# Kernel tuning notes

Hardware: AMD Instinct MI355X
Metric: run time of the kernel (lower is better)

The kernel has to match this reference:

```python
import jax, jax.numpy as jnp
import numpy as np

B, L, H, NH, DH, V, NL = 256, 100, 384, 12, 32, 30000, 6
FF = 4 * H


def _gelu(x):
    c = np.sqrt(2.0 / np.pi).astype(np.float32)
    return x * (0.5 * (1.0 + jnp.tanh(c * (x + 0.044715 * x ** 3))))


def _norm(X, g, b):
    mu = jnp.mean(X, axis=2, keepdims=True)
    var = jnp.var(X, axis=2, ddof=1, keepdims=True)  # torch.var is unbiased
    return g * ((X - mu) / jnp.sqrt(var + 1e-8)) + b


def setup_inputs():
    key = jax.random.key(0)
    ks = jax.random.split(key, 24)
    s = 0.02
    return {
        'x': jax.random.randint(ks[0], (B, L), 0, V, dtype=jnp.int32),
        'seg': jax.random.randint(ks[1], (B, L), 0, 3, dtype=jnp.int32),
        'tok_emb': jax.random.uniform(ks[2], (V, H), jnp.float32, -s, s),
        'seg_emb': jax.random.uniform(ks[3], (3, H), jnp.float32, -s, s),
        'pos_emb': jax.random.normal(ks[4], (L, H), jnp.float32) * 0.05,
        'Wq': jax.random.normal(ks[5], (NL, H, H), jnp.float32) * np.sqrt(2.0 / H).astype(np.float32),
        'bq': jnp.zeros((NL, H), jnp.float32),
        'Wk': jax.random.normal(ks[6], (NL, H, H), jnp.float32) * np.sqrt(2.0 / H).astype(np.float32),
        'bk': jnp.zeros((NL, H), jnp.float32),
        'Wv': jax.random.normal(ks[7], (NL, H, H), jnp.float32) * np.sqrt(2.0 / H).astype(np.float32),
        'bv': jnp.zeros((NL, H), jnp.float32),
        'Wo': jax.random.normal(ks[8], (NL, H, H), jnp.float32) * np.sqrt(2.0 / (2 * H)).astype(np.float32),
        'bo': jnp.zeros((NL, H), jnp.float32),
        'g1': jnp.ones((NL,), jnp.float32),
        'be1': jnp.zeros((NL,), jnp.float32),
        'W1': jax.random.normal(ks[9], (NL, H, FF), jnp.float32) * np.sqrt(2.0 / (H + FF)).astype(np.float32),
        'b1': jnp.zeros((NL, FF), jnp.float32),
        'W2': jax.random.normal(ks[10], (NL, FF, H), jnp.float32) * np.sqrt(2.0 / (H + FF)).astype(np.float32),
        'b2': jnp.zeros((NL, H), jnp.float32),
        'g2': jnp.ones((NL,), jnp.float32),
        'be2': jnp.zeros((NL,), jnp.float32),
        'dropout': 0,
    }


def _encoder_layer(h, pad_mask, nonpad, Wq, bq, Wk, bk, Wv, bv, Wo, bo, g1, be1, W1, b1, W2, b2, g2, be2):
    # --- multi-head self-attention (interleaved head split, as in source) ---
    q = (h @ Wq + bq).reshape(B, L, DH, NH).transpose(3, 0, 1, 2)  # (NH,B,L,DH)
    k = (h @ Wk + bk).reshape(B, L, DH, NH).transpose(3, 0, 3 - 1, 1)  # placeholder
    k = (h @ Wk + bk).reshape(B, L, DH, NH).transpose(3, 0, 2, 1)      # (NH,B,DH,L)
    v = (h @ Wv + bv).reshape(B, L, DH, NH).transpose(3, 0, 1, 2)      # (NH,B,L,DH)
    scale = 1.0 / np.sqrt(H).astype(np.float32)  # d_k = de.shape[-1] = hidden_dim!
    e = jnp.einsum('hbld,hbdm->hblm', q, k) * scale                    # (NH,B,L,L)
    e = jnp.where(pad_mask[None], -1e10, e)
    alpha = jax.nn.softmax(e, axis=-1)
    heads = jnp.einsum('hblm,hbmd->hbld', alpha, v)                    # (NH,B,L,DH)
    a = heads.transpose(1, 2, 0, 3).reshape(B, L, H)  # cat over heads on feature dim
    attn = _norm(a @ Wo + bo + h, g1, be1)
    attn = attn * nonpad
    # --- FFN ---
    f = _gelu(attn @ W1 + b1)
    f = f @ W2 + b2
    out = _norm(f + attn, g2, be2)
    return out * nonpad


def reference(x, seg, tok_emb, seg_emb, pos_emb, Wq, bq, Wk, bk, Wv, bv, Wo, bo,
              g1, be1, W1, b1, W2, b2, g2, be2, dropout):
    pad_mask = (x == 0)[:, None, :] * jnp.ones((1, L, 1), bool)  # (B,L,L)
    nonpad = (x != 0).astype(jnp.float32)[:, :, None]            # (B,L,1), bcast over H
    h = tok_emb[x] + seg_emb[seg] + pos_emb[None, :L]
    h = h * nonpad
    acc = h  # cumulative-sum skip connections: input_i = x_i + ... + x_1
    out = h
    for i in range(NL):
        out = _encoder_layer(acc, pad_mask, nonpad,
                             Wq[i], bq[i], Wk[i], bk[i], Wv[i], bv[i], Wo[i], bo[i],
                             g1[i], be1[i], W1[i], b1[i], W2[i], b2[i], g2[i], be2[i])
        acc = acc + out
    return out
```

## Files before the change

### kernel.cpp

```cpp
#include <hip/hip_runtime.h>
#include <hip/hip_bf16.h>
#include <math.h>

#define B_  256
#define L_  100
#define H_  384
#define NH_ 12
#define DH_ 32
#define NL_ 6
#define FF_ 1536
#define M_  (B_*L_)
#define QKVN 1152

#define OFF_Q  0
#define OFF_K  294912
#define OFF_V  589824
#define OFF_WO 884736
#define OFF_W1 1179648
#define OFF_W2 2359296

typedef __attribute__((ext_vector_type(8))) short short8;
typedef __attribute__((ext_vector_type(4))) float f32x4;

#define GLOBAL_AS __attribute__((address_space(1)))
#define LDS_AS    __attribute__((address_space(3)))

__device__ __forceinline__ void gload_lds16(const void* g, void* l) {
    __builtin_amdgcn_global_load_lds((const GLOBAL_AS void*)g, (LDS_AS void*)l, 16, 0, 0);
}

__device__ __forceinline__ void split2(float v, __hip_bfloat16& hi, __hip_bfloat16& lo) {
    hi = __float2bfloat16(v);
    lo = __float2bfloat16(v - __bfloat162float(hi));
}

__device__ __forceinline__ unsigned short f2b(float v) {
    __hip_bfloat16 h = __float2bfloat16(v);
    return *(unsigned short*)&h;
}

__global__ void embed_kernel(const int* __restrict__ x, const int* __restrict__ seg,
                             const float* __restrict__ tok, const float* __restrict__ sege,
                             const float* __restrict__ pos,
                             __hip_bfloat16* __restrict__ acc2) {
    int idx = blockIdx.x * blockDim.x + threadIdx.x;
    if (idx >= M_ * H_) return;
    int m = idx / H_;
    int f = idx - m * H_;
    int t = x[m];
    int s = seg[m];
    int l = m % L_;
    float v = tok[t * H_ + f] + sege[s * H_ + f] + pos[l * H_ + f];
    v = (t != 0) ? v : 0.0f;
    __hip_bfloat16 h, lo;
    split2(v, h, lo);
    acc2[(size_t)m * (2 * H_) + f]      = h;
    acc2[(size_t)m * (2 * H_) + H_ + f] = lo;
}

__global__ void transpose_all_kernel(const float* __restrict__ Wq, const float* __restrict__ Wk,
        const float* __restrict__ Wv, const float* __restrict__ Wo,
        const float* __restrict__ W1, const float* __restrict__ W2,
        __hip_bfloat16* __restrict__ wTL) {
    __shared__ float tile[32][33];
    int bid = blockIdx.x;
    const float* src;
    __hip_bfloat16* dst;
    int K, N, nx, tix, perm = 0;
    if (bid < 432) {
        int m = bid / 144; tix = bid % 144;
        src = (m == 0) ? Wq : (m == 1 ? Wk : Wv);
        dst = wTL + (m == 0 ? OFF_Q : (m == 1 ? OFF_K : OFF_V));
        K = 384; N = 384; nx = 12; perm = 1;
    } else if (bid < 576) {
        tix = bid - 432; src = Wo; dst = wTL + OFF_WO; K = 384; N = 384; nx = 12;
    } else if (bid < 1152) {
        tix = bid - 576; src = W1; dst = wTL + OFF_W1; K = 384; N = 1536; nx = 48;
    } else {
        tix = bid - 1152; src = W2; dst = wTL + OFF_W2; K = 1536; N = 384; nx = 12;
    }
    int n0 = (tix % nx) * 32, k0 = (tix / nx) * 32;
    int tx = threadIdx.x, ty = threadIdx.y;
    #pragma unroll
    for (int i = ty; i < 32; i += 8)
        tile[i][tx] = src[(size_t)(k0 + i) * N + (n0 + tx)];
    __syncthreads();
    #pragma unroll
    for (int i = ty; i < 32; i += 8) {
        float v = tile[tx][i];
        __hip_bfloat16 h, lo;
        split2(v, h, lo);
        int j = n0 + i;
        int jo = perm ? ((j % 12) * 32 + j / 12) : j;
        dst[(size_t)jo * (2 * K) + (k0 + tx)]     = h;
        dst[(size_t)jo * (2 * K) + K + (k0 + tx)] = lo;
    }
}

__global__ void bias_concat_kernel(const float* __restrict__ bq, const float* __restrict__ bk,
                                   const float* __restrict__ bv, float* __restrict__ out) {
    int i = blockIdx.x * 256 + threadIdx.x;
    if (i >= NL_ * QKVN) return;
    int l = i / QKVN, jp = i - l * QKVN;
    int t = jp / 384, r = jp % 384;
    int h = r >> 5, d = r & 31;
    int j = d * 12 + h;
    float v = (t == 0) ? bq[l * 384 + j] : (t == 1 ? bk[l * 384 + j] : bv[l * 384 + j]);
    out[i] = v;
}

template <int TAG, int BIG, int OMODE, int MODEK, int ACT>
__global__ __launch_bounds__(BIG ? 512 : 256) void gemm_bf16_kernel(
        const __hip_bfloat16* __restrict__ A2,
        const __hip_bfloat16* __restrict__ Wt2,
        const float* __restrict__ bias,
        void* __restrict__ outp,
        int N, int K, int nbx) {
    constexpr int BM = BIG ? 256 : 128;
    __shared__ __hip_bfloat16 As[2][BM * 32];
    __shared__ __hip_bfloat16 Bs[2][128 * 32];
    int t = threadIdx.x;
    int lane = t & 63, wv = t >> 6;
    int wm = wv >> 1, wn = wv & 1;

    int nwg = gridDim.x;
    int q8 = nwg >> 3, r8 = nwg & 7;
    int xcd = blockIdx.x & 7, off = blockIdx.x >> 3;
    int swz = (xcd < r8 ? xcd * (q8 + 1) : r8 * (q8 + 1) + (xcd - r8) * q8) + off;
    int bn = (swz % nbx) * 128;
    int bm = (swz / nbx) * BM;

    const int KstA = (MODEK == 2) ? K : 2 * K;
    const int KstW = 2 * K;
    const int Kend = (MODEK == 0) ? 3 * K : 2 * K;
    f32x4 acc[4][4] = {};

    int sr   = t >> 2;
    int sswz = (t & 3) ^ ((t >> 2) & 3) ^ ((t >> 4) & 3);
    const __hip_bfloat16* a_src = A2 + (size_t)(bm + sr) * KstA + sswz * 8;
    const __hip_bfloat16* b_src = Wt2 + (size_t)(bn + sr) * KstW + sswz * 8;

    int slotp = (lane >> 4) ^ (lane & 3) ^ ((lane >> 2) & 3);
    int aOff = (wm * 64 + (lane & 15)) * 32 + slotp * 8;
    int bOff = (wn * 64 + (lane & 15)) * 32 + slotp * 8;

#define STAGE(buf, ak, wk) do { \
        gload_lds16(a_src + (ak), &As[buf][wv * 512]); \
        gload_lds16(a_src + (size_t)(BM / 2) * KstA + (ak), &As[buf][(BM / 2) * 32 + wv * 512]); \
        gload_lds16(b_src + (wk), &Bs[buf][wv * 512]); \
        if (!BIG) gload_lds16(b_src + (size_t)64 * KstW + (wk), &Bs[buf][2048 + wv * 512]); \
    } while (0)

#define KOFFS(k0, ak, wk) do { \
        if (MODEK == 0) { ak = ((k0) < K) ? (k0) : (k0) - K; wk = ((k0) < 2 * K) ? (k0) : (k0) - 2 * K; } \
        else if (MODEK == 1) { ak = (k0); wk = ((k0) < K) ? (k0) : (k0) - K; } \
        else { ak = ((k0) < K) ? (k0) : (k0) - K; wk = (k0); } \
    } while (0)

    int nt = Kend >> 5;
    STAGE(0, 0, 0);
    __syncthreads();
    int cur = 0;
    for (int ti = 0; ti < nt; ++ti) {
        int k1 = (ti + 1) << 5;
        if (ti + 1 < nt) {
            int ak, wk;
            KOFFS(k1, ak, wk);
            STAGE(cur ^ 1, ak, wk);
        }
        short8 af[4], bf[4];
        #pragma unroll
        for (int m = 0; m < 4; ++m) af[m] = *(const short8*)(&As[cur][aOff + m * 512]);
        #pragma unroll
        for (int n = 0; n < 4; ++n) bf[n] = *(const short8*)(&Bs[cur][bOff + n * 512]);
        #pragma unroll
        for (int m = 0; m < 4; ++m)
            #pragma unroll
            for (int n = 0; n < 4; ++n)
                acc[m][n] = __builtin_amdgcn_mfma_f32_16x16x32_bf16(af[m], bf[n], acc[m][n], 0, 0, 0);
        __syncthreads();
        cur ^= 1;
    }
#undef STAGE
#undef KOFFS

    int colBase = bn + wn * 64 + (lane & 15);
    int rowBase = bm + wm * 64 + (lane >> 4) * 4;
    const float c0 = 0.7978845608f;
    #pragma unroll
    for (int n = 0; n < 4; ++n) {
        int c = colBase + n * 16;
        float bvv = bias[c];
        #pragma unroll
        for (int m = 0; m < 4; ++m) {
            int r0 = rowBase + m * 16;
            #pragma unroll
            for (int r = 0; r < 4; ++r) {
                float v = acc[m][n][r] + bvv;
                if (ACT == 1) {
                    float u = c0 * (v + 0.044715f * v * v * v);
                    v = v / (1.0f + __expf(-2.0f * u));
                }
                size_t row = (size_t)(r0 + r);
                if (OMODE == 0) {
                    ((float*)outp)[row * N + c] = v;
                } else {
                    ((__hip_bfloat16*)outp)[row * N + c] = __float2bfloat16(v);
                }
            }
        }
    }
}

__global__ __launch_bounds__(256) void attn_kernel(const __hip_bfloat16* __restrict__ qkvP,
        const int* __restrict__ x, __hip_bfloat16* __restrict__ a2) {
    __shared__ unsigned short qs[112][32];
    __shared__ unsigned short ks[128][32];
    __shared__ unsigned short vst[32][136];
    __shared__ unsigned short ps[112][136];
    __shared__ int xb[128];
    int t = threadIdx.x;
    int lane = t & 63, wv = t >> 6;
    int b = blockIdx.x / NH_;
    int nh = blockIdx.x % NH_;
    const __hip_bfloat16* base = qkvP + (size_t)b * L_ * QKVN;

    for (int i = t; i < 576; i += 256) {
        int d = i / 18, w = i % 18;
        ((int*)vst)[d * 68 + 50 + w] = 0;
    }
    for (int i = t; i < 128; i += 256) xb[i] = (i < L_) ? x[b * L_ + i] : 0;

    {
        int r16 = lane >> 2, s = lane & 3;
        for (int i = wv; i < 7; i += 4) {
            int row = i * 16 + r16;
            int sp = s ^ (row & 3) ^ ((row >> 2) & 3);
            gload_lds16(base + (size_t)row * QKVN + nh * 32 + sp * 8, &qs[i * 16][0]);
        }
        for (int i = wv; i < 8; i += 4) {
            int row = i * 16 + r16;
            int sp = s ^ (row & 3) ^ ((row >> 2) & 3);
            gload_lds16(base + (size_t)row * QKVN + 384 + nh * 32 + sp * 8, &ks[i * 16][0]);
        }
    }
    if (t < 200) {
        int kv = t >> 1, d0 = (t & 1) * 16;
        const __hip_bfloat16* vsrc = base + (size_t)kv * QKVN + 768 + nh * 32 + d0;
        short8 v0 = *(const short8*)vsrc;
        short8 v1 = *(const short8*)(vsrc + 8);
        #pragma unroll
        for (int j = 0; j < 8; ++j) {
            vst[d0 + j][kv]     = (unsigned short)v0[j];
            vst[d0 + 8 + j][kv] = (unsigned short)v1[j];
        }
    }
    __syncthreads();

    const float scale = 1.0f / sqrtf((float)H_);
    int n = lane & 15, g = lane >> 4;

    for (int rt = wv; rt < 7; rt += 4) {
        int arow = rt * 16 + n;
        int asp = (g ^ (arow & 3) ^ ((arow >> 2) & 3)) * 8;
        short8 aq = *(const short8*)&qs[arow][asp];
        f32x4 s8[8];
        #pragma unroll
        for (int ct = 0; ct < 8; ++ct) {
            int brow = ct * 16 + n;
            int bsp = (g ^ (brow & 3) ^ ((brow >> 2) & 3)) * 8;
            short8 bk = *(const short8*)&ks[brow][bsp];
            f32x4 z = {0.0f, 0.0f, 0.0f, 0.0f};
            s8[ct] = __builtin_amdgcn_mfma_f32_16x16x32_bf16(aq, bk, z, 0, 0, 0);
        }
        #pragma unroll
        for (int ct = 0; ct < 8; ++ct) {
            int col = ct * 16 + n;
            int xv = xb[col];
            #pragma unroll
            for (int r = 0; r < 4; ++r) {
                float v = s8[ct][r] * scale;
                v = (xv == 0) ? -1e10f : v;
                v = (col >= L_) ? -INFINITY : v;
                s8[ct][r] = v;
            }
        }
        float sm[4];
        #pragma unroll
        for (int r = 0; r < 4; ++r) {
            float m = s8[0][r];
            #pragma unroll
            for (int ct = 1; ct < 8; ++ct) m = fmaxf(m, s8[ct][r]);
            m = fmaxf(m, __shfl_xor(m, 1, 16));
            m = fmaxf(m, __shfl_xor(m, 2, 16));
            m = fmaxf(m, __shfl_xor(m, 4, 16));
            m = fmaxf(m, __shfl_xor(m, 8, 16));
            float s = 0.0f;
            #pragma unroll
            for (int ct = 0; ct < 8; ++ct) {
                float p = __expf(s8[ct][r] - m);
                s8[ct][r] = p;
                s += p;
            }
            s += __shfl_xor(s, 1, 16);
            s += __shfl_xor(s, 2, 16);
            s += __shfl_xor(s, 4, 16);
            s += __shfl_xor(s, 8, 16);
            sm[r] = s;
        }
        int prow = rt * 16 + g * 4;
        #pragma unroll
        for (int ct = 0; ct < 8; ++ct) {
            int col = ct * 16 + n;
            #pragma unroll
            for (int r = 0; r < 4; ++r)
                ps[prow + r][col] = f2b(s8[ct][r]);
        }
        f32x4 o0 = {0.0f, 0.0f, 0.0f, 0.0f}, o1 = o0;
        #pragma unroll
        for (int kt = 0; kt < 4; ++kt) {
            short8 pa = *(const short8*)&ps[rt * 16 + n][kt * 32 + g * 8];
            short8 b0 = *(const short8*)&vst[n][kt * 32 + g * 8];
            short8 b1 = *(const short8*)&vst[16 + n][kt * 32 + g * 8];
            o0 = __builtin_amdgcn_mfma_f32_16x16x32_bf16(pa, b0, o0, 0, 0, 0);
            o1 = __builtin_amdgcn_mfma_f32_16x16x32_bf16(pa, b1, o1, 0, 0, 0);
        }
        #pragma unroll
        for (int r = 0; r < 4; ++r) {
            int lrow = prow + r;
            if (lrow < L_) {
                size_t row = (size_t)b * L_ + lrow;
                float inv = 1.0f / sm[r];
                __hip_bfloat16 h, lo;
                float v0 = o0[r] * inv;
                split2(v0, h, lo);
                a2[row * (2 * H_) + nh * DH_ + n]      = h;
                a2[row * (2 * H_) + H_ + nh * DH_ + n] = lo;
                float v1 = o1[r] * inv;
                split2(v1, h, lo);
                a2[row * (2 * H_) + nh * DH_ + 16 + n]      = h;
                a2[row * (2 * H_) + H_ + nh * DH_ + 16 + n] = lo;
            }
        }
    }
}

template <int MODE>
__global__ __launch_bounds__(128) void ln_kernel(
        const float* __restrict__ Xf,
        const __hip_bfloat16* __restrict__ R2,
        const int* __restrict__ x,
        const float* __restrict__ gp, const float* __restrict__ bp, int layer,
        float* __restrict__ Yf,
        __hip_bfloat16* __restrict__ Y2,
        __hip_bfloat16* __restrict__ acc2) {
    int row = blockIdx.x;
    int tid = threadIdx.x;
    size_t b1 = (size_t)row * H_;
    size_t b2 = (size_t)row * (2 * H_);

    float v[3];
    #pragma unroll
    for (int j = 0; j < 3; ++j) {
        int f = tid + j * 128;
        float r = __bfloat162float(R2[b2 + f]) + __bfloat162float(R2[b2 + H_ + f]);
        v[j] = Xf[b1 + f] + r;
    }

    __shared__ float red[2];
    float s = v[0] + v[1] + v[2];
    #pragma unroll
    for (int off = 32; off > 0; off >>= 1) s += __shfl_down(s, off);
    if ((tid & 63) == 0) red[tid >> 6] = s;
    __syncthreads();
    float mu = (red[0] + red[1]) * (1.0f / 384.0f);
    __syncthreads();

    float d[3];
    float qq = 0.0f;
    #pragma unroll
    for (int j = 0; j < 3; ++j) { d[j] = v[j] - mu; qq += d[j] * d[j]; }
    #pragma unroll
    for (int off = 32; off > 0; off >>= 1) qq += __shfl_down(qq, off);
    if ((tid & 63) == 0) red[tid >> 6] = qq;
    __syncthreads();
    float var = (red[0] + red[1]) * (1.0f / 383.0f);
    float rstd = rsqrtf(var + 1e-8f);

    float g = gp[layer], bb = bp[layer];
    float np_ = (x[row] != 0) ? 1.0f : 0.0f;
    #pragma unroll
    for (int j = 0; j < 3; ++j) {
        int f = tid + j * 128;
        float y = (g * (d[j] * rstd) + bb) * np_;
        if (MODE == 0) {
            __hip_bfloat16 h, lo;
            split2(y, h, lo);
            Y2[b2 + f]      = h;
            Y2[b2 + H_ + f] = lo;
        } else {
            Yf[b1 + f] = y;
            float a = __bfloat162float(acc2[b2 + f]) + __bfloat162float(acc2[b2 + H_ + f]) + y;
            __hip_bfloat16 h, lo;
            split2(a, h, lo);
            acc2[b2 + f]      = h;
            acc2[b2 + H_ + f] = lo;
        }
    }
}

extern "C" void kernel_launch(void* const* d_in, const int* in_sizes, int n_in,
                              void* d_out, int out_size, void* d_ws, size_t ws_size,
                              hipStream_t stream) {
    const int*   x    = (const int*)d_in[0];
    const int*   seg  = (const int*)d_in[1];
    const float* tok  = (const float*)d_in[2];
    const float* sege = (const float*)d_in[3];
    const float* pos  = (const float*)d_in[4];
    const float* Wq   = (const float*)d_in[5];
    const float* bq   = (const float*)d_in[6];
    const float* Wk   = (const float*)d_in[7];
    const float* bk   = (const float*)d_in[8];
    const float* Wv   = (const float*)d_in[9];
    const float* bv   = (const float*)d_in[10];
    const float* Wo   = (const float*)d_in[11];
    const float* bo   = (const float*)d_in[12];
    const float* g1   = (const float*)d_in[13];
    const float* be1  = (const float*)d_in[14];
    const float* W1   = (const float*)d_in[15];
    const float* b1   = (const float*)d_in[16];
    const float* W2   = (const float*)d_in[17];
    const float* b2   = (const float*)d_in[18];
    const float* g2   = (const float*)d_in[19];
    const float* be2  = (const float*)d_in[20];

    char* p = (char*)d_ws;
    __hip_bfloat16* wTL  = (__hip_bfloat16*)p; p += 7077888;
    __hip_bfloat16* acc2 = (__hip_bfloat16*)p; p += 39321600;
    __hip_bfloat16* bE2  = (__hip_bfloat16*)p; p += 39321600;
    float* qkvb          = (float*)p;          p += 27648;
    char* pool           = p;
    __hip_bfloat16* qkvP = (__hip_bfloat16*)pool;
    __hip_bfloat16* bA2  = (__hip_bfloat16*)(pool + 58982400);
    float*          woF  = (float*)pool;
    __hip_bfloat16* f2   = (__hip_bfloat16*)pool;
    float* out = (float*)d_out;

    bias_concat_kernel<<<dim3((NL_ * QKVN + 255) / 256), dim3(256), 0, stream>>>(bq, bk, bv, qkvb);
    embed_kernel<<<dim3((M_ * H_ + 255) / 256), dim3(256), 0, stream>>>(x, seg, tok, sege, pos, acc2);

    for (int l = 0; l < NL_; ++l) {
        transpose_all_kernel<<<dim3(1728), dim3(32, 8), 0, stream>>>(
            Wq + (size_t)l * H_ * H_, Wk + (size_t)l * H_ * H_, Wv + (size_t)l * H_ * H_,
            Wo + (size_t)l * H_ * H_, W1 + (size_t)l * H_ * FF_, W2 + (size_t)l * FF_ * H_, wTL);

        const float* bol = bo + (size_t)l * H_;
        const float* b1l = b1 + (size_t)l * FF_;
        const float* b2l = b2 + (size_t)l * H_;

        gemm_bf16_kernel<0, 1, 2, 0, 0><<<dim3((QKVN / 128) * (M_ / 256)), dim3(512), 0, stream>>>(
            acc2, wTL + OFF_Q, qkvb + (size_t)l * QKVN, qkvP, QKVN, H_, QKVN / 128);
        attn_kernel<<<dim3(B_ * NH_), dim3(256), 0, stream>>>(qkvP, x, bA2);
        gemm_bf16_kernel<1, 0, 0, 0, 0><<<dim3((H_ / 128) * (M_ / 128)), dim3(256), 0, stream>>>(
            bA2, wTL + OFF_WO, bol, woF, H_, H_, H_ / 128);
        ln_kernel<0><<<dim3(M_), dim3(128), 0, stream>>>(
            woF, acc2, x, g1, be1, l, nullptr, bE2, nullptr);
        gemm_bf16_kernel<2, 1, 2, 0, 1><<<dim3((FF_ / 128) * (M_ / 256)), dim3(512), 0, stream>>>(
            bE2, wTL + OFF_W1, b1l, f2, FF_, H_, FF_ / 128);
        gemm_bf16_kernel<3, 0, 0, 2, 0><<<dim3((H_ / 128) * (M_ / 128)), dim3(256), 0, stream>>>(
            f2, wTL + OFF_W2, b2l, out, H_, FF_, H_ / 128);
        ln_kernel<1><<<dim3(M_), dim3(128), 0, stream>>>(
            out, bE2, x, g2, be2, l, out, nullptr, acc2);
    }
}
```

Measured before the change: 2.545 ms.

## Triple-buffer GEMM LDS staging with explicit vmcnt waits and MFMA priority

The bf16 GEMM's double-buffered LDS pipeline becomes a three-stage ring. Global-to-LDS loads are issued two K-tiles ahead, and a hand-counted s_waitcnt vmcnt plus a raw s_barrier replaces __syncthreads. The MFMA block is wrapped in s_setprio so compute waves get issue priority while loads are in flight. The aim is to hide global load latency better, at the cost of more LDS per block (possible occupancy loss). The MODEK==1 offset branch is also dropped, which changes offsets if that mode is instantiated.

Result: no change. 2.522 ms (-0.9%).

```diff
diff --git a/kernel.cpp b/kernel.cpp
--- a/kernel.cpp
+++ b/kernel.cpp
@@ -38,6 +38,8 @@
     __hip_bfloat16 h = __float2bfloat16(v);
     return *(unsigned short*)&h;
 }
+
+#define VMW(N) asm volatile("s_waitcnt vmcnt(" #N ")" ::: "memory")
 
 __global__ void embed_kernel(const int* __restrict__ x, const int* __restrict__ seg,
                              const float* __restrict__ tok, const float* __restrict__ sege,
@@ -117,8 +119,8 @@
         void* __restrict__ outp,
         int N, int K, int nbx) {
     constexpr int BM = BIG ? 256 : 128;
-    __shared__ __hip_bfloat16 As[2][BM * 32];
-    __shared__ __hip_bfloat16 Bs[2][128 * 32];
+    __shared__ __hip_bfloat16 As[3][BM * 32];
+    __shared__ __hip_bfloat16 Bs[3][128 * 32];
     int t = threadIdx.x;
     int lane = t & 63, wv = t >> 6;
     int wm = wv >> 1, wn = wv & 1;
@@ -153,40 +155,52 @@
 
 #define KOFFS(k0, ak, wk) do { \
         if (MODEK == 0) { ak = ((k0) < K) ? (k0) : (k0) - K; wk = ((k0) < 2 * K) ? (k0) : (k0) - 2 * K; } \
-        else if (MODEK == 1) { ak = (k0); wk = ((k0) < K) ? (k0) : (k0) - K; } \
         else { ak = ((k0) < K) ? (k0) : (k0) - K; wk = (k0); } \
     } while (0)
 
     int nt = Kend >> 5;
-    STAGE(0, 0, 0);
-    __syncthreads();
-    int cur = 0;
+    {
+        int ak, wk;
+        KOFFS(0, ak, wk);
+        STAGE(0, ak, wk);
+        KOFFS(32, ak, wk);
+        STAGE(1, ak, wk);
+    }
+    int c0 = 0, c1 = 1, c2 = 2;
     for (int ti = 0; ti < nt; ++ti) {
-        int k1 = (ti + 1) << 5;
-        if (ti + 1 < nt) {
+        if (ti + 2 < nt) {
+            int k2 = (ti + 2) << 5;
             int ak, wk;
-            KOFFS(k1, ak, wk);
-            STAGE(cur ^ 1, ak, wk);
-        }
+            KOFFS(k2, ak, wk);
+            STAGE(c2, ak, wk);
+            if (BIG) { VMW(6); } else { VMW(8); }
+        } else if (ti + 2 == nt) {
+            if (BIG) { VMW(3); } else { VMW(4); }
+        } else {
+            VMW(0);
+        }
+        __builtin_amdgcn_s_barrier();
         short8 af[4], bf[4];
         #pragma unroll
-        for (int m = 0; m < 4; ++m) af[m] = *(const short8*)(&As[cur][aOff + m * 512]);
-        #pragma unroll
-        for (int n = 0; n < 4; ++n) bf[n] = *(const short8*)(&Bs[cur][bOff + n * 512]);
+        for (int m = 0; m < 4; ++m) af[m] = *(const short8*)(&As[c0][aOff + m * 512]);
+        #pragma unroll
+        for (int n = 0; n < 4; ++n) bf[n] = *(const short8*)(&Bs[c0][bOff + n * 512]);
+        __builtin_amdgcn_s_setprio(1);
         #pragma unroll
         for (int m = 0; m < 4; ++m)
             #pragma unroll
             for (int n = 0; n < 4; ++n)
                 acc[m][n] = __builtin_amdgcn_mfma_f32_16x16x32_bf16(af[m], bf[n], acc[m][n], 0, 0, 0);
-        __syncthreads();
-        cur ^= 1;
+        __builtin_amdgcn_s_setprio(0);
+        __builtin_amdgcn_s_barrier();
+        int tmp = c0; c0 = c1; c1 = c2; c2 = tmp;
     }
 #undef STAGE
 #undef KOFFS
 
     int colBase = bn + wn * 64 + (lane & 15);
     int rowBase = bm + wm * 64 + (lane >> 4) * 4;
-    const float c0 = 0.7978845608f;
+    const float c0f = 0.7978845608f;
     #pragma unroll
     for (int n = 0; n < 4; ++n) {
         int c = colBase + n * 16;
@@ -198,7 +212,7 @@
             for (int r = 0; r < 4; ++r) {
                 float v = acc[m][n][r] + bvv;
                 if (ACT == 1) {
-                    float u = c0 * (v + 0.044715f * v * v * v);
+                    float u = c0f * (v + 0.044715f * v * v * v);
                     v = v / (1.0f + __expf(-2.0f * u));
                 }
                 size_t row = (size_t)(r0 + r);
```
